# Performance work log

Measured on AMD Instinct MI355X. Metric: run time of the kernel, lower is better.

Reference implementation:

```python
import jax, jax.numpy as jnp
import numpy as np

N = 65536   # total sentences
B = 8192    # number of bags (ragged scopes)
C = 1024    # class_dim
R = 100     # rel_num


def setup_inputs() -> dict:
    key = jax.random.key(0)
    k1, k2, k3, k4 = jax.random.split(key, 4)
    X = jax.random.normal(k1, (N, C), jnp.float32)            # post-fc1 sentence reps
    Constraints = jax.random.normal(k2, (R, C), jnp.float32)  # post-fc2 constraint reps
    W = jax.random.normal(k3, (R, C), jnp.float32) * 0.02     # classifier weight
    b = jnp.zeros((R,), jnp.float32)                           # classifier bias
    # ragged scopes: random cut points -> contiguous [start, end) per bag
    rng = np.random.default_rng(0)
    cuts = np.sort(rng.choice(np.arange(1, N), B - 1, replace=False))
    starts = np.concatenate([[0], cuts])
    ends = np.concatenate([cuts, [N]])
    X_Scope = jnp.asarray(np.stack([starts, ends], axis=1), jnp.int32)  # [B, 2]
    X_Rel = jax.random.randint(k4, (B,), 0, R, jnp.int32)               # [B]
    return dict(X=X, Constraints=Constraints, W=W, b=b, X_Scope=X_Scope, X_Rel=X_Rel)


def reference(X, Constraints, W, b, X_Scope, X_Rel):
    n, _ = X.shape
    nb = X_Scope.shape[0]
    # map each sentence to its (contiguous) bag via scope starts
    starts = X_Scope[:, 0]
    seg = jnp.searchsorted(starts, jnp.arange(n, dtype=starts.dtype), side='right') - 1  # [N]
    # per-sentence attention logit against its bag's relation constraint
    Con = Constraints[X_Rel]                                   # [B, C]
    scores = jnp.einsum('nc,nc->n', X, Con[seg])               # [N]
    # numerically-stable per-bag softmax
    m = jax.ops.segment_max(scores, seg, num_segments=nb)      # [B]
    e = jnp.exp(scores - m[seg])                               # [N]
    denom = jax.ops.segment_sum(e, seg, num_segments=nb)       # [B]
    w = e / denom[seg]                                         # [N]
    # attention-weighted bag pooling
    bag = jax.ops.segment_sum(w[:, None] * X, seg, num_segments=nb)  # [B, C]
    # classifier (dropout is identity at eval)
    return bag @ W.T + b                                       # [B, R]
```

## Files before the change

kernel.cpp:

```cpp
#include <hip/hip_runtime.h>
#include <math.h>

#define CDIM 1024
#define RDIM 100
#define NBAGS 8192

typedef float floatx4 __attribute__((ext_vector_type(4)));
typedef short bf16x8 __attribute__((ext_vector_type(8)));

__device__ __forceinline__ float dot4(float4 a, float4 b) {
    return a.x * b.x + a.y * b.y + a.z * b.z + a.w * b.w;
}

__device__ __forceinline__ unsigned short f2bf(float f) {
    unsigned int u = __builtin_bit_cast(unsigned int, f);
    u += 0x7FFFu + ((u >> 16) & 1u);
    return (unsigned short)(u >> 16);
}

__global__ __launch_bounds__(256) void bag_softmax_kernel(
    const float* __restrict__ X,
    const float* __restrict__ Constraints,
    const int* __restrict__ scope,
    const int* __restrict__ rel,
    const float* __restrict__ W,
    unsigned short* __restrict__ bagbuf,
    unsigned short* __restrict__ Wbf)
{
    const int lane = threadIdx.x & 63;
    const int w    = threadIdx.x >> 6;

    if (blockIdx.x >= NBAGS) {
        const int rr = blockIdx.x - NBAGS;
        const int t  = threadIdx.x;
        float4 v = *(const float4*)(W + (size_t)rr * CDIM + t * 4);
        ushort4 o;
        o.x = f2bf(v.x); o.y = f2bf(v.y); o.z = f2bf(v.z); o.w = f2bf(v.w);
        *(ushort4*)(Wbf + (size_t)rr * CDIM + t * 4) = o;
        return;
    }

    __shared__ float4 lds_acc[4][256];
    __shared__ float  lds_m[4];
    __shared__ float  lds_d[4];

    const int bag = blockIdx.x;
    const int s = scope[2 * bag];
    const int e = scope[2 * bag + 1];
    const int r = rel[bag];

    const float4* conp = (const float4*)(Constraints + (size_t)r * CDIM);
    const float4 c0 = conp[lane];
    const float4 c1 = conp[lane + 64];
    const float4 c2 = conp[lane + 128];
    const float4 c3 = conp[lane + 192];

    float4 a0 = {0.f, 0.f, 0.f, 0.f};
    float4 a1 = {0.f, 0.f, 0.f, 0.f};
    float4 a2 = {0.f, 0.f, 0.f, 0.f};
    float4 a3 = {0.f, 0.f, 0.f, 0.f};
    float m = -INFINITY;
    float denom = 0.f;

    int row = s + w;
    if (row < e) {
        const float4* xp = (const float4*)(X + (size_t)row * CDIM);
        float4 A0 = xp[lane];
        float4 A1 = xp[lane + 64];
        float4 A2 = xp[lane + 128];
        float4 A3 = xp[lane + 192];

        for (; row < e; row += 4) {
            const int nxt = (row + 4 < e) ? (row + 4) : row;
            const float4* np = (const float4*)(X + (size_t)nxt * CDIM);
            float4 B0 = np[lane];
            float4 B1 = np[lane + 64];
            float4 B2 = np[lane + 128];
            float4 B3 = np[lane + 192];
            __builtin_amdgcn_sched_barrier(0);

            float p = dot4(A0, c0) + dot4(A1, c1) + dot4(A2, c2) + dot4(A3, c3);
            p += __shfl_xor(p, 1);
            p += __shfl_xor(p, 2);
            p += __shfl_xor(p, 4);
            p += __shfl_xor(p, 8);
            p += __shfl_xor(p, 16);
            p += __shfl_xor(p, 32);

            const float newm = fmaxf(m, p);
            const float corr = __expf(m - newm);
            const float wgt  = __expf(p - newm);
            denom = fmaf(denom, corr, wgt);
            a0.x = fmaf(a0.x, corr, wgt * A0.x); a0.y = fmaf(a0.y, corr, wgt * A0.y);
            a0.z = fmaf(a0.z, corr, wgt * A0.z); a0.w = fmaf(a0.w, corr, wgt * A0.w);
            a1.x = fmaf(a1.x, corr, wgt * A1.x); a1.y = fmaf(a1.y, corr, wgt * A1.y);
            a1.z = fmaf(a1.z, corr, wgt * A1.z); a1.w = fmaf(a1.w, corr, wgt * A1.w);
            a2.x = fmaf(a2.x, corr, wgt * A2.x); a2.y = fmaf(a2.y, corr, wgt * A2.y);
            a2.z = fmaf(a2.z, corr, wgt * A2.z); a2.w = fmaf(a2.w, corr, wgt * A2.w);
            a3.x = fmaf(a3.x, corr, wgt * A3.x); a3.y = fmaf(a3.y, corr, wgt * A3.y);
            a3.z = fmaf(a3.z, corr, wgt * A3.z); a3.w = fmaf(a3.w, corr, wgt * A3.w);
            m = newm;

            A0 = B0; A1 = B1; A2 = B2; A3 = B3;
        }
    }

    if (lane == 0) { lds_m[w] = m; lds_d[w] = denom; }
    lds_acc[w][lane]       = a0;
    lds_acc[w][lane + 64]  = a1;
    lds_acc[w][lane + 128] = a2;
    lds_acc[w][lane + 192] = a3;
    __syncthreads();

    const int t = threadIdx.x;
    const float m0 = lds_m[0], m1 = lds_m[1], m2 = lds_m[2], m3 = lds_m[3];
    const float ms = fmaxf(fmaxf(m0, m1), fmaxf(m2, m3));
    const float f0 = __expf(m0 - ms);
    const float f1 = __expf(m1 - ms);
    const float f2 = __expf(m2 - ms);
    const float f3 = __expf(m3 - ms);
    const float dn = f0 * lds_d[0] + f1 * lds_d[1] + f2 * lds_d[2] + f3 * lds_d[3];
    const float inv = 1.0f / dn;

    const float4 v0 = lds_acc[0][t];
    const float4 v1 = lds_acc[1][t];
    const float4 v2 = lds_acc[2][t];
    const float4 v3 = lds_acc[3][t];
    const float ox = (f0 * v0.x + f1 * v1.x + f2 * v2.x + f3 * v3.x) * inv;
    const float oy = (f0 * v0.y + f1 * v1.y + f2 * v2.y + f3 * v3.y) * inv;
    const float oz = (f0 * v0.z + f1 * v1.z + f2 * v2.z + f3 * v3.z) * inv;
    const float ow = (f0 * v0.w + f1 * v1.w + f2 * v2.w + f3 * v3.w) * inv;

    ushort4 o;
    o.x = f2bf(ox); o.y = f2bf(oy); o.z = f2bf(oz); o.w = f2bf(ow);
    *(ushort4*)(bagbuf + (size_t)bag * CDIM + t * 4) = o;
}

__global__ __launch_bounds__(128) void bag_gemm_mfma(
    const unsigned short* __restrict__ bagbuf,
    const unsigned short* __restrict__ Wbf,
    const float* __restrict__ bias,
    float* __restrict__ out)
{
    const int wid  = threadIdx.x >> 6;
    const int lane = threadIdx.x & 63;
    const int bag0 = (blockIdx.x * 2 + wid) * 16;
    const int ln15 = lane & 15;
    const int koff = (lane >> 4) * 8;

    floatx4 acc[7];
    #pragma unroll
    for (int t = 0; t < 7; ++t) acc[t] = (floatx4){0.f, 0.f, 0.f, 0.f};

    const unsigned short* aRow = bagbuf + (size_t)(bag0 + ln15) * CDIM + koff;
    const int rB = ln15;

    for (int kc = 0; kc < CDIM / 32; ++kc) {
        const int k0 = kc * 32;
        const bf16x8 a = *(const bf16x8*)(aRow + k0);

        #pragma unroll
        for (int t = 0; t < 7; ++t) {
            const int r = t * 16 + rB;
            bf16x8 b = (bf16x8)0;
            if (r < RDIM) {
                b = *(const bf16x8*)(Wbf + (size_t)r * CDIM + k0 + koff);
            }
            acc[t] = __builtin_amdgcn_mfma_f32_16x16x32_bf16(a, b, acc[t], 0, 0, 0);
        }
    }

    const int mbase = (lane >> 4) * 4;
    #pragma unroll
    for (int t = 0; t < 7; ++t) {
        const int r = t * 16 + rB;
        if (r < RDIM) {
            const float bv = bias[r];
            #pragma unroll
            for (int reg = 0; reg < 4; ++reg) {
                const int bag = bag0 + mbase + reg;
                out[(size_t)bag * RDIM + r] = acc[t][reg] + bv;
            }
        }
    }
}

extern "C" void kernel_launch(void* const* d_in, const int* in_sizes, int n_in,
                              void* d_out, int out_size, void* d_ws, size_t ws_size,
                              hipStream_t stream) {
    const float* X    = (const float*)d_in[0];
    const float* Con  = (const float*)d_in[1];
    const float* W    = (const float*)d_in[2];
    const float* bias = (const float*)d_in[3];
    const int* scope  = (const int*)d_in[4];
    const int* rel    = (const int*)d_in[5];
    float* out = (float*)d_out;

    unsigned short* bagbuf = (unsigned short*)d_ws;
    unsigned short* Wbf    = bagbuf + (size_t)NBAGS * CDIM;

    bag_softmax_kernel<<<NBAGS + RDIM, 256, 0, stream>>>(X, Con, scope, rel, W, bagbuf, Wbf);
    bag_gemm_mfma<<<NBAGS / 32, 128, 0, stream>>>(bagbuf, Wbf, bias, out);
}
```

Measured before the change: 79.11 us.

## Split GEMM K dimension across four waves with LDS reduction

```diff
diff --git a/kernel.cpp b/kernel.cpp
--- a/kernel.cpp
+++ b/kernel.cpp
@@ -136,32 +136,34 @@
     *(ushort4*)(bagbuf + (size_t)bag * CDIM + t * 4) = o;
 }
 
-__global__ __launch_bounds__(128) void bag_gemm_mfma(
+__global__ __launch_bounds__(256) void bag_gemm_mfma(
     const unsigned short* __restrict__ bagbuf,
     const unsigned short* __restrict__ Wbf,
     const float* __restrict__ bias,
     float* __restrict__ out)
 {
-    const int wid  = threadIdx.x >> 6;
+    const int q    = threadIdx.x >> 6;
     const int lane = threadIdx.x & 63;
-    const int bag0 = (blockIdx.x * 2 + wid) * 16;
+    const int bag0 = blockIdx.x * 16;
     const int ln15 = lane & 15;
     const int koff = (lane >> 4) * 8;
 
+    __shared__ floatx4 lds[4][7][64];
+
     floatx4 acc[7];
     #pragma unroll
     for (int t = 0; t < 7; ++t) acc[t] = (floatx4){0.f, 0.f, 0.f, 0.f};
 
     const unsigned short* aRow = bagbuf + (size_t)(bag0 + ln15) * CDIM + koff;
-    const int rB = ln15;
-
-    for (int kc = 0; kc < CDIM / 32; ++kc) {
-        const int k0 = kc * 32;
+
+    #pragma unroll
+    for (int i = 0; i < 8; ++i) {
+        const int k0 = (q * 8 + i) * 32;
         const bf16x8 a = *(const bf16x8*)(aRow + k0);
 
         #pragma unroll
         for (int t = 0; t < 7; ++t) {
-            const int r = t * 16 + rB;
+            const int r = t * 16 + ln15;
             bf16x8 b = (bf16x8)0;
             if (r < RDIM) {
                 b = *(const bf16x8*)(Wbf + (size_t)r * CDIM + k0 + koff);
@@ -170,17 +172,26 @@
         }
     }
 
-    const int mbase = (lane >> 4) * 4;
-    #pragma unroll
-    for (int t = 0; t < 7; ++t) {
-        const int r = t * 16 + rB;
+    #pragma unroll
+    for (int t = 0; t < 7; ++t) lds[q][t][lane] = acc[t];
+    __syncthreads();
+
+    #pragma unroll
+    for (int p = threadIdx.x; p < 448; p += 256) {
+        const int t    = p >> 6;
+        const int slot = p & 63;
+        const int r    = t * 16 + (slot & 15);
         if (r < RDIM) {
+            floatx4 s = lds[0][t][slot];
+            s += lds[1][t][slot];
+            s += lds[2][t][slot];
+            s += lds[3][t][slot];
             const float bv = bias[r];
-            #pragma unroll
-            for (int reg = 0; reg < 4; ++reg) {
-                const int bag = bag0 + mbase + reg;
-                out[(size_t)bag * RDIM + r] = acc[t][reg] + bv;
-            }
+            const int bagr = bag0 + (slot >> 4) * 4;
+            out[(size_t)(bagr + 0) * RDIM + r] = s[0] + bv;
+            out[(size_t)(bagr + 1) * RDIM + r] = s[1] + bv;
+            out[(size_t)(bagr + 2) * RDIM + r] = s[2] + bv;
+            out[(size_t)(bagr + 3) * RDIM + r] = s[3] + bv;
         }
     }
 }
@@ -200,5 +211,5 @@
     unsigned short* Wbf    = bagbuf + (size_t)NBAGS * CDIM;
 
     bag_softmax_kernel<<<NBAGS + RDIM, 256, 0, stream>>>(X, Con, scope, rel, W, bagbuf, Wbf);
-    bag_gemm_mfma<<<NBAGS / 32, 128, 0, stream>>>(bagbuf, Wbf, bias, out);
-}
+    bag_gemm_mfma<<<NBAGS / 16, 256, 0, stream>>>(bagbuf, Wbf, bias, out);
+}
```

After: 72.26 us. 8.7% less time.
